# Kernel optimization log

Hardware: AMD Instinct MI355X
Metric: run time of the kernel (lower is better)

Reference implementation:

```python
import jax, jax.numpy as jnp
import numpy as np

N_CHAINS, L, N, D, K, H, FF = 8192, 128, 100000, 256, 8, 4, 1024
LN_EPS = 1e-5  # torch LayerNorm default
EPS = 1e-8     # module eps for mean-pool denom


def _ln(x, g, b):
    mu = jnp.mean(x, axis=-1, keepdims=True)
    var = jnp.mean((x - mu) ** 2, axis=-1, keepdims=True)
    return (x - mu) * jax.lax.rsqrt(var + LN_EPS) * g + b


def setup_inputs() -> dict:
    key = jax.random.key(0)
    ks = jax.random.split(key, 24)
    s = 1.0 / np.sqrt(D)
    inp = {
        "v": jax.random.normal(ks[0], (N, D), jnp.float32),
        "batch_idx": jax.random.randint(ks[1], (N_CHAINS, L), 0, N),
        "mask": jax.random.uniform(ks[2], (N_CHAINS, L)) > 0.5,
        "count": jax.random.randint(ks[3], (N_CHAINS,), 0, 128).astype(jnp.float32),
        "rank_scores": jax.random.normal(ks[4], (N_CHAINS, L), jnp.float32),
        "pos_embed": jnp.zeros((1, K, D), jnp.float32),
        "w_qkv": jax.random.normal(ks[5], (3 * D, D), jnp.float32) * s,
        "b_qkv": jnp.zeros((3 * D,), jnp.float32),
        "w_o": jax.random.normal(ks[6], (D, D), jnp.float32) * s,
        "b_o": jnp.zeros((D,), jnp.float32),
        "ln1_g": jnp.ones((D,), jnp.float32),
        "ln1_b": jnp.zeros((D,), jnp.float32),
        "ln2_g": jnp.ones((D,), jnp.float32),
        "ln2_b": jnp.zeros((D,), jnp.float32),
        "w_ff1": jax.random.normal(ks[7], (FF, D), jnp.float32) * s,
        "b_ff1": jnp.zeros((FF,), jnp.float32),
        "w_ff2": jax.random.normal(ks[8], (D, FF), jnp.float32) / np.sqrt(FF),
        "b_ff2": jnp.zeros((D,), jnp.float32),
        "w_out1": jax.random.normal(ks[9], (FF, D + 1), jnp.float32) * s,
        "b_out1": jnp.zeros((FF,), jnp.float32),
        "w_out2": jax.random.normal(ks[10], (D, FF), jnp.float32) / np.sqrt(FF),
        "b_out2": jnp.zeros((D,), jnp.float32),
    }
    return inp


def reference(v, batch_idx, mask, count, rank_scores, pos_embed, w_qkv, b_qkv,
              w_o, b_o, ln1_g, ln1_b, ln2_g, ln2_b, w_ff1, b_ff1, w_ff2, b_ff2,
              w_out1, b_out1, w_out2, b_out2):
    neg = jnp.finfo(jnp.float32).min
    # --- top-k relevance selection among masked positions ---
    masked_scores = jnp.where(mask, rank_scores.astype(jnp.float32), neg)
    _, top_idx = jax.lax.top_k(masked_scores, K)                # [n, K]
    picked = jnp.take_along_axis(mask, top_idx, axis=1)
    sortable = jnp.where(picked, top_idx, L)                     # sentinel L
    sortable = jnp.sort(sortable, axis=1)
    picked = sortable < L
    safe_idx = jnp.where(picked, sortable, 0)                    # [n, K]
    # gather-pack: v[batch_idx][safe_idx] == v[batch_idx gathered at safe_idx]
    member_idx = jnp.take_along_axis(batch_idx, safe_idx, axis=1)
    packed = v[member_idx] * picked[..., None].astype(v.dtype)   # [n, K, D]

    x = packed + pos_embed[:, :K, :]
    kpm = ~picked                                                # True = pad
    empty = jnp.all(kpm, axis=1)
    kpm = kpm.at[:, 0].set(jnp.where(empty, False, kpm[:, 0]))

    # --- one pre-LN transformer encoder layer (gelu, dropout=0) ---
    dh = D // H
    h = _ln(x, ln1_g, ln1_b)
    qkv = h @ w_qkv.T + b_qkv                                    # [n, K, 3D]
    q, k, val = jnp.split(qkv, 3, axis=-1)
    q = q.reshape(-1, K, H, dh)
    k = k.reshape(-1, K, H, dh)
    val = val.reshape(-1, K, H, dh)
    scores = jnp.einsum('bqhd,bkhd->bhqk', q, k) / np.sqrt(dh)
    scores = jnp.where(kpm[:, None, None, :], neg, scores)
    attn = jax.nn.softmax(scores, axis=-1)
    o = jnp.einsum('bhqk,bkhd->bqhd', attn, val).reshape(-1, K, D)
    x = x + (o @ w_o.T + b_o)
    h = _ln(x, ln2_g, ln2_b)
    x = x + jax.nn.gelu(h @ w_ff1.T + b_ff1, approximate=False) @ w_ff2.T + b_ff2

    # --- masked mean pool + log-count feature + MLP head ---
    pf = picked.astype(x.dtype)
    denom = jnp.clip(jnp.sum(pf, axis=1, keepdims=True), EPS, None)
    pooled = jnp.sum(x * pf[..., None], axis=1) / denom
    pooled = jnp.where(jnp.any(picked, axis=1, keepdims=True), pooled, 0.0)
    feat = jnp.concatenate([pooled, jnp.log1p(count.astype(x.dtype))[:, None]], axis=-1)
    return jax.nn.gelu(feat @ w_out1.T + b_out1, approximate=False) @ w_out2.T + b_out2
```

## Files before the change

kernel.cpp:

```cpp
#include <hip/hip_runtime.h>


#define DIM   256
#define LSEQ  128
#define KTOK  8

typedef __bf16 bf16x8 __attribute__((ext_vector_type(8)));
typedef float  f32x4  __attribute__((ext_vector_type(4)));
typedef unsigned short u16x8 __attribute__((ext_vector_type(8)));

__device__ __forceinline__ f32x4 mfma16(bf16x8 a, bf16x8 b, f32x4 c) {
  return __builtin_amdgcn_mfma_f32_16x16x32_bf16(a, b, c, 0, 0, 0);
}

__device__ __forceinline__ unsigned short f2bf(float f) {
  union { __bf16 h; unsigned short u; } cv;
  cv.h = (__bf16)f;
  return cv.u;
}

__device__ __forceinline__ unsigned pack2bf(float a, float b) {
  union { __bf16 h2[2]; unsigned u; } cv;
  cv.h2[0] = (__bf16)a; cv.h2[1] = (__bf16)b;
  return cv.u;
}

__device__ __forceinline__ float gelu_fast(float x) {
  const float x2 = x * x;
  const float y = x * __builtin_fmaf(0.0356774081f, x2, 0.7978845608f);
  const float e = __expf(2.f * y);
  const float r = __builtin_amdgcn_rcpf(e + 1.f);
  const float t = __builtin_fmaf(-2.f, r, 1.f);
  return 0.5f * x * (1.f + t);
}

__device__ __forceinline__ float rsum8(float v) {
  v += __shfl_xor(v, 1);
  v += __shfl_xor(v, 2);
  v += __shfl_xor(v, 4);
  return v;
}

union U4 { unsigned u[4]; bf16x8 v; };

__device__ __forceinline__ void gload16(const unsigned short* g, unsigned short* lds_uniform) {
  auto gp = reinterpret_cast<const __attribute__((address_space(1))) unsigned*>(
      reinterpret_cast<uintptr_t>(g));
  auto lp = reinterpret_cast<__attribute__((address_space(3))) unsigned*>(
      (unsigned)reinterpret_cast<uintptr_t>(lds_uniform));
  __builtin_amdgcn_global_load_lds(gp, lp, 16, 0, 0);
}

struct Stage32 { u16x8 r[4]; };
__device__ __forceinline__ void stage_load(Stage32& st, const unsigned short* __restrict__ g, int tid) {
  #pragma unroll
  for (int i = 0; i < 4; ++i) st.r[i] = *(const u16x8*)&g[(tid + i * 512) * 8];
}
__device__ __forceinline__ void stage_commit(const Stage32& st, unsigned short* l, int tid) {
  #pragma unroll
  for (int i = 0; i < 4; ++i) *(u16x8*)&l[(tid + i * 512) * 8] = st.r[i];
}

__device__ __forceinline__ void pack_region(
    const float* __restrict__ src, unsigned short* __restrict__ dst,
    int g, int KC, int Ksrc, int Klim)
{
  const int ln = g & 63;
  const int t = g >> 6;
  const int s = t % KC;
  const int ntile = t / KC;
  const int row = ntile * 16 + (ln & 15);
  const int c0 = s * 32 + (ln >> 4) * 8;
  u16x8 o;
  #pragma unroll
  for (int j = 0; j < 8; ++j) {
    float val = (c0 + j < Klim) ? src[(long)row * Ksrc + c0 + j] : 0.f;
    o[j] = f2bf(val);
  }
  *(u16x8*)&dst[(long)g * 8] = o;
}

__device__ __forceinline__ void pack_region_kmaj(
    const float* __restrict__ src, unsigned short* __restrict__ dst,
    int g, int NT, int Ksrc)
{
  const int ln = g & 63;
  const int t = g >> 6;
  const int ntile = t % NT;
  const int s = t / NT;
  const int row = ntile * 16 + (ln & 15);
  const int c0 = s * 32 + (ln >> 4) * 8;
  u16x8 o;
  #pragma unroll
  for (int j = 0; j < 8; ++j) o[j] = f2bf(src[(long)row * Ksrc + c0 + j]);
  *(u16x8*)&dst[(long)g * 8] = o;
}

#define PREP_GROUPS 172032
__global__ __launch_bounds__(256) void k_prep(
    const float* __restrict__ wqkv, const float* __restrict__ wo,
    const float* __restrict__ wff1, const float* __restrict__ wff2,
    const float* __restrict__ wout1, const float* __restrict__ wout2,
    unsigned short* __restrict__ oq, unsigned short* __restrict__ oo,
    unsigned short* __restrict__ of1, unsigned short* __restrict__ of2,
    unsigned short* __restrict__ oo1, unsigned short* __restrict__ oo2)
{
  int g = blockIdx.x * 256 + threadIdx.x;
  if (g < 24576) { pack_region(wqkv, oq, g, 8, 256, 256); return; }
  g -= 24576;
  if (g < 8192)  { pack_region(wo, oo, g, 8, 256, 256); return; }
  g -= 8192;
  if (g < 32768) { pack_region(wff1, of1, g, 8, 256, 256); return; }
  g -= 32768;
  if (g < 32768) { pack_region_kmaj(wff2, of2, g, 16, 1024); return; }
  g -= 32768;
  if (g < 40960) { pack_region(wout1, oo1, g, 10, 257, 257); return; }
  g -= 40960;
  if (g < 32768) { pack_region_kmaj(wout2, oo2, g, 16, 1024); }
}

__global__ __launch_bounds__(256) void k_sel(
    const float* __restrict__ v, const int* __restrict__ batch_idx,
    const int* __restrict__ mask, const float* __restrict__ rank_scores,
    const float* __restrict__ pos_embed,
    const float* __restrict__ ln1g, const float* __restrict__ ln1b,
    float* __restrict__ X, unsigned short* __restrict__ H1p,
    int* __restrict__ NPICK)
{
  const int c = blockIdx.x;
  const int tid = threadIdx.x;
  __shared__ int s_mem[KTOK];
  __shared__ int s_np;

  if (tid < 64) {
    const int l = tid;
    unsigned long long key[2];
    #pragma unroll
    for (int t = 0; t < 2; ++t) {
      int p = l + 64 * t;
      int mk = mask[c * LSEQ + p];
      float s = rank_scores[c * LSEQ + p];
      unsigned u = __float_as_uint(s);
      u = (u & 0x80000000u) ? ~u : (u | 0x80000000u);
      unsigned long long kk =
          ((unsigned long long)u << 32) | (unsigned long long)(0xFFFFFFFFu - (unsigned)p);
      key[t] = mk ? kk : 0ull;
    }
    int w[KTOK];
    #pragma unroll
    for (int r = 0; r < KTOK; ++r) w[r] = 0x7FFFFFFF;
    int np = 0;
    for (int r = 0; r < KTOK; ++r) {
      unsigned long long best = key[0] > key[1] ? key[0] : key[1];
      for (int off = 32; off > 0; off >>= 1) {
        unsigned long long o = __shfl_xor(best, off, 64);
        if (o > best) best = o;
      }
      if (best == 0ull) break;
      int idx = (int)(0xFFFFFFFFu - (unsigned)(best & 0xFFFFFFFFull));
      w[np++] = idx;
      if (key[0] == best) key[0] = 0ull;
      if (key[1] == best) key[1] = 0ull;
    }
    #pragma unroll
    for (int a = 0; a < KTOK - 1; ++a)
      #pragma unroll
      for (int b2 = 0; b2 < KTOK - 1 - a; ++b2) {
        int x0 = w[b2], x1 = w[b2 + 1];
        w[b2] = min(x0, x1); w[b2 + 1] = max(x0, x1);
      }
    if (l < KTOK) s_mem[l] = (l < np) ? batch_idx[c * LSEQ + w[l]] : -1;
    if (l == 0) { s_np = np; NPICK[c] = np; }
  }
  __syncthreads();

  const int np = s_np;
  const int j = tid >> 5, q = tid & 31;
  const int r = s_mem[j];
  const float4* v4  = (const float4*)v;
  const float4* pe4 = (const float4*)pos_embed;
  float4* X4 = (float4*)X;

  float4 xv[2];
  #pragma unroll
  for (int rep = 0; rep < 2; ++rep) {
    const int f = 2 * q + rep;
    float4 pe = pe4[j * 64 + f];
    float4 val = make_float4(0.f, 0.f, 0.f, 0.f);
    if (j < np) val = v4[(long)r * 64 + f];
    xv[rep].x = val.x + pe.x; xv[rep].y = val.y + pe.y;
    xv[rep].z = val.z + pe.z; xv[rep].w = val.w + pe.w;
    X4[((long)c * KTOK + j) * 64 + f] = xv[rep];
  }
  float sum = 0.f, ss = 0.f;
  #pragma unroll
  for (int rep = 0; rep < 2; ++rep) {
    sum += xv[rep].x + xv[rep].y + xv[rep].z + xv[rep].w;
    ss  += xv[rep].x * xv[rep].x + xv[rep].y * xv[rep].y
         + xv[rep].z * xv[rep].z + xv[rep].w * xv[rep].w;
  }
  #pragma unroll
  for (int off = 1; off <= 16; off <<= 1) {
    sum += __shfl_xor(sum, off); ss += __shfl_xor(ss, off);
  }
  const float mu = sum * (1.f / 256.f);
  const float var = ss * (1.f / 256.f) - mu * mu;
  const float rstd = rsqrtf(var + 1e-5f);
  const int t = c * KTOK + j;
  const int mtile = t >> 4, lr = t & 15;
  const int s = q >> 2, lq = q & 3;
  u16x8 o;
  const int col = q * 8;
  o[0] = f2bf((xv[0].x - mu) * rstd * ln1g[col + 0] + ln1b[col + 0]);
  o[1] = f2bf((xv[0].y - mu) * rstd * ln1g[col + 1] + ln1b[col + 1]);
  o[2] = f2bf((xv[0].z - mu) * rstd * ln1g[col + 2] + ln1b[col + 2]);
  o[3] = f2bf((xv[0].w - mu) * rstd * ln1g[col + 3] + ln1b[col + 3]);
  o[4] = f2bf((xv[1].x - mu) * rstd * ln1g[col + 4] + ln1b[col + 4]);
  o[5] = f2bf((xv[1].y - mu) * rstd * ln1g[col + 5] + ln1b[col + 5]);
  o[6] = f2bf((xv[1].z - mu) * rstd * ln1g[col + 6] + ln1b[col + 6]);
  o[7] = f2bf((xv[1].w - mu) * rstd * ln1g[col + 7] + ln1b[col + 7]);
  *(u16x8*)&H1p[((long)(mtile * 8 + s) * 64 + lq * 16 + lr) * 8] = o;
}

__global__ __launch_bounds__(512, 4) void k_qkv(
    const unsigned short* __restrict__ H1p, unsigned short* __restrict__ QKVp,
    const unsigned short* __restrict__ wqp, const float* __restrict__ bqkv)
{
  __shared__ unsigned short buf[16384];
  __shared__ unsigned short sT[8 * 16 * 72];
  const int tid = threadIdx.x;
  const int wv = tid >> 6, ln = tid & 63;
  const int lr = ln & 15, lq = ln >> 4;
  const int mtile = blockIdx.x * 8 + wv;
  const f32x4 vzero = {0.f, 0.f, 0.f, 0.f};
  unsigned short* sTw = &sT[wv * 1152];

  bf16x8 af[8];
  #pragma unroll
  for (int s = 0; s < 8; ++s)
    af[s] = *(const bf16x8*)&H1p[((long)(mtile * 8 + s) * 64 + ln) * 8];

  Stage32 st;
  stage_load(st, wqp, tid);
  for (int c = 0; c < 12; ++c) {
    stage_commit(st, buf, tid);
    __syncthreads();
    if (c < 11) stage_load(st, wqp + (c + 1) * 16384, tid);
    f32x4 acc[4];
    #pragma unroll
    for (int nt = 0; nt < 4; ++nt) acc[nt] = vzero;
    #pragma unroll
    for (int s = 0; s < 8; ++s) {
      #pragma unroll
      for (int nt = 0; nt < 4; ++nt) {
        bf16x8 b = *(const bf16x8*)&buf[(nt * 8 + s) * 512 + ln * 8];
        acc[nt] = mfma16(af[s], b, acc[nt]);
      }
    }
    #pragma unroll
    for (int nt = 0; nt < 4; ++nt) {
      const float bias = bqkv[c * 64 + nt * 16 + lr];
      #pragma unroll
      for (int reg = 0; reg < 4; ++reg)
        sTw[(lq * 4 + reg) * 72 + nt * 16 + lr] = f2bf(acc[nt][reg] + bias);
    }
    const int r8 = ln >> 3, cg = ln & 7;
    #pragma unroll
    for (int h = 0; h < 2; ++h) {
      const int tok = h * 8 + r8;
      u16x8 vv = *(const u16x8*)&sTw[tok * 72 + cg * 8];
      *(u16x8*)&QKVp[((long)(mtile * 16 + tok)) * 768 + c * 64 + cg * 8] = vv;
    }
    __syncthreads();
  }
}

#define SKV 520

__global__ __launch_bounds__(128) void k_attn(
    const unsigned short* __restrict__ QKVp, const int* __restrict__ NPICK,
    unsigned short* __restrict__ Op)
{
  __shared__ unsigned short sKV[32 * SKV];
  __shared__ int s_np[4];
  const int tid = threadIdx.x;
  const int blk = blockIdx.x;
  if (tid < 4) s_np[tid] = NPICK[blk * 4 + tid];
  for (int i = tid; i < 2048; i += 128) {
    const int r = i >> 6, u = i & 63;
    *(u16x8*)&sKV[r * SKV + u * 8] =
        *(const u16x8*)&QKVp[((long)blk * 32 + r) * 768 + 256 + u * 8];
  }
  const int c = tid >> 5, hh = (tid >> 3) & 3, qi = tid & 7;
  const int qrow = c * 8 + qi;
  bf16x8 qv[8];
  #pragma unroll
  for (int dc = 0; dc < 8; ++dc)
    qv[dc] = *(const bf16x8*)&QKVp[((long)blk * 32 + qrow) * 768 + hh * 64 + dc * 8];
  __syncthreads();

  const int natt = max(1, s_np[c]);
  float sc[8];
  #pragma unroll
  for (int j = 0; j < 8; ++j) sc[j] = -1e30f;
  for (int j = 0; j < natt; ++j) {
    float d = 0.f;
    #pragma unroll
    for (int dc = 0; dc < 8; ++dc) {
      bf16x8 kv = *(const bf16x8*)&sKV[(c * 8 + j) * SKV + hh * 64 + dc * 8];
      #pragma unroll
      for (int e = 0; e < 8; ++e) d += (float)qv[dc][e] * (float)kv[e];
    }
    sc[j] = d * 0.125f;
  }
  float mx = -1e30f;
  #pragma unroll
  for (int j = 0; j < 8; ++j) mx = fmaxf(mx, sc[j]);
  float pr[8]; float ssum = 0.f;
  #pragma unroll
  for (int j = 0; j < 8; ++j) {
    float e = (j < natt) ? __expf(sc[j] - mx) : 0.f;
    pr[j] = e; ssum += e;
  }
  const float inv = 1.f / ssum;
  const int t = blk * 32 + qrow;
  const int mt = t >> 4, lrt = t & 15;
  #pragma unroll
  for (int dc = 0; dc < 8; ++dc) {
    float o8[8] = {0.f,0.f,0.f,0.f,0.f,0.f,0.f,0.f};
    for (int j = 0; j < natt; ++j) {
      const float pj = pr[j] * inv;
      bf16x8 vv = *(const bf16x8*)&sKV[(c * 8 + j) * SKV + 256 + hh * 64 + dc * 8];
      #pragma unroll
      for (int e = 0; e < 8; ++e) o8[e] += pj * (float)vv[e];
    }
    u16x8 o;
    #pragma unroll
    for (int e = 0; e < 8; ++e) o[e] = f2bf(o8[e]);
    const int s = hh * 2 + (dc >> 2), lqt = dc & 3;
    *(u16x8*)&Op[((long)(mt * 8 + s) * 64 + lqt * 16 + lrt) * 8] = o;
  }
}

__global__ __launch_bounds__(512, 4) void k_oproj(
    const unsigned short* __restrict__ Op, float* __restrict__ X,
    const unsigned short* __restrict__ wop, const float* __restrict__ bo,
    const float* __restrict__ ln2g, const float* __restrict__ ln2b,
    unsigned short* __restrict__ H2p)
{
  __shared__ unsigned short buf[16384];
  __shared__ float sTf[8 * 16 * 68];
  const int tid = threadIdx.x;
  const int wv = tid >> 6, ln = tid & 63;
  const int lr = ln & 15, lq = ln >> 4;
  const int mtile = blockIdx.x * 8 + wv;
  const f32x4 vzero = {0.f, 0.f, 0.f, 0.f};
  float* sTw = &sTf[wv * 1088];

  bf16x8 af[8];
  #pragma unroll
  for (int s = 0; s < 8; ++s)
    af[s] = *(const bf16x8*)&Op[((long)(mtile * 8 + s) * 64 + ln) * 8];

  const int r4 = ln >> 2, g4 = ln & 3;
  float lsum = 0.f, lss = 0.f;

  Stage32 st;
  stage_load(st, wop, tid);
  for (int c = 0; c < 4; ++c) {
    stage_commit(st, buf, tid);
    __syncthreads();
    if (c < 3) stage_load(st, wop + (c + 1) * 16384, tid);
    f32x4 acc[4];
    #pragma unroll
    for (int nt = 0; nt < 4; ++nt) acc[nt] = vzero;
    #pragma unroll
    for (int s = 0; s < 8; ++s) {
      #pragma unroll
      for (int nt = 0; nt < 4; ++nt) {
        bf16x8 b = *(const bf16x8*)&buf[(nt * 8 + s) * 512 + ln * 8];
        acc[nt] = mfma16(af[s], b, acc[nt]);
      }
    }
    #pragma unroll
    for (int nt = 0; nt < 4; ++nt) {
      const float bias = bo[c * 64 + nt * 16 + lr];
      #pragma unroll
      for (int reg = 0; reg < 4; ++reg)
        sTw[(lq * 4 + reg) * 68 + nt * 16 + lr] = acc[nt][reg] + bias;
    }
    #pragma unroll
    for (int it = 0; it < 4; ++it) {
      const int gi = it * 4 + g4;
      f32x4 vv = *(const f32x4*)&sTw[r4 * 68 + gi * 4];
      float4* xp = (float4*)&X[((long)(mtile * 16 + r4)) * DIM + c * 64 + gi * 4];
      float4 old = *xp;
      old.x += vv[0]; old.y += vv[1]; old.z += vv[2]; old.w += vv[3];
      *xp = old;
      lsum += old.x + old.y + old.z + old.w;
      lss  += old.x * old.x + old.y * old.y + old.z * old.z + old.w * old.w;
    }
    __syncthreads();
  }
  lsum += __shfl_xor(lsum, 1); lss += __shfl_xor(lss, 1);
  lsum += __shfl_xor(lsum, 2); lss += __shfl_xor(lss, 2);
  const float mu = lsum * (1.f / 256.f);
  const float rstd = rsqrtf(lss * (1.f / 256.f) - mu * mu + 1e-5f);
  const int row = mtile * 16 + r4;
  #pragma unroll
  for (int i = 0; i < 8; ++i) {
    const int q = i * 4 + g4;
    const float4 x0 = *(const float4*)&X[(long)row * DIM + q * 8];
    const float4 x1 = *(const float4*)&X[(long)row * DIM + q * 8 + 4];
    const float4 g0 = *(const float4*)&ln2g[q * 8];
    const float4 g1 = *(const float4*)&ln2g[q * 8 + 4];
    const float4 b0 = *(const float4*)&ln2b[q * 8];
    const float4 b1 = *(const float4*)&ln2b[q * 8 + 4];
    u16x8 o;
    o[0] = f2bf((x0.x - mu) * rstd * g0.x + b0.x);
    o[1] = f2bf((x0.y - mu) * rstd * g0.y + b0.y);
    o[2] = f2bf((x0.z - mu) * rstd * g0.z + b0.z);
    o[3] = f2bf((x0.w - mu) * rstd * g0.w + b0.w);
    o[4] = f2bf((x1.x - mu) * rstd * g1.x + b1.x);
    o[5] = f2bf((x1.y - mu) * rstd * g1.y + b1.y);
    o[6] = f2bf((x1.z - mu) * rstd * g1.z + b1.z);
    o[7] = f2bf((x1.w - mu) * rstd * g1.w + b1.w);
    *(u16x8*)&H2p[((long)(mtile * 8 + (q >> 2)) * 64 + (q & 3) * 16 + r4) * 8] = o;
  }
}

__global__ __launch_bounds__(256, 2) void k_ff(
    const float* __restrict__ X, const unsigned short* __restrict__ H2p,
    const unsigned short* __restrict__ w1p, const unsigned short* __restrict__ w2p,
    const float* __restrict__ bff1, const float* __restrict__ bff2,
    const int* __restrict__ NPICK, const float* __restrict__ count,
    unsigned short* __restrict__ Fp)
{
  __shared__ unsigned short buf[2][8192];
  __shared__ unsigned short Gs[16384];
  __shared__ float Pxf[4096];
  const int tid = threadIdx.x;
  const int wv = tid >> 6, ln = tid & 63;
  const int lr = ln & 15, lq = ln >> 4;
  const int blk = blockIdx.x;
  const int mtA = blk * 8 + wv * 2, mtB = mtA + 1;
  const f32x4 vzero = {0.f, 0.f, 0.f, 0.f};

  const int sub = (ln >> 3) & 1;
  const int npcAl = NPICK[mtA * 2 + sub];
  const int npcBl = NPICK[mtB * 2 + sub];
  const float mTA = ((ln & 7) < npcAl) ? 1.f : 0.f;
  const float mTB = ((ln & 7) < npcBl) ? 1.f : 0.f;
  const int chA = wv * 4 + sub;
  const int chB = wv * 4 + 2 + sub;

  bf16x8 afA[8], afB[8];
  #pragma unroll
  for (int s = 0; s < 8; ++s) {
    afA[s] = *(const bf16x8*)&H2p[((long)(mtA * 8 + s) * 64 + ln) * 8];
    afB[s] = *(const bf16x8*)&H2p[((long)(mtB * 8 + s) * 64 + ln) * 8];
  }

  #pragma unroll
  for (int c = 0; c < 4; ++c) {
    const int off = (c * 256 + wv * 64) * 8;
    gload16(w1p + off + ln * 8, &buf[0][off]);
  }
  __syncthreads();

  for (int i = 0; i < 32; ++i) {
    const unsigned short* bcur = buf[i & 1];
    if (i < 31) {
      unsigned short* bnxt = buf[(i + 1) & 1];
      #pragma unroll
      for (int c = 0; c < 4; ++c) {
        const int off = (c * 256 + wv * 64) * 8;
        gload16(w1p + (long)(i + 1) * 8192 + off + ln * 8, &bnxt[off]);
      }
    }
    f32x4 gaA[2], gaB[2];
    #pragma unroll
    for (int nt = 0; nt < 2; ++nt) { gaA[nt] = vzero; gaB[nt] = vzero; }
    #pragma unroll
    for (int s = 0; s < 8; ++s) {
      #pragma unroll
      for (int nt = 0; nt < 2; ++nt) {
        const bf16x8 w1f = *(const bf16x8*)&bcur[(nt * 8 + s) * 512 + ln * 8];
        gaA[nt] = mfma16(w1f, afA[s], gaA[nt]);
        gaB[nt] = mfma16(w1f, afB[s], gaB[nt]);
      }
    }
    float sA[2][4], sB[2][4];
    #pragma unroll
    for (int nt = 0; nt < 2; ++nt) {
      const float4 b4 = *(const float4*)&bff1[i * 32 + nt * 16 + lq * 4];
      sA[nt][0] = rsum8(gelu_fast(gaA[nt][0] + b4.x) * mTA);
      sA[nt][1] = rsum8(gelu_fast(gaA[nt][1] + b4.y) * mTA);
      sA[nt][2] = rsum8(gelu_fast(gaA[nt][2] + b4.z) * mTA);
      sA[nt][3] = rsum8(gelu_fast(gaA[nt][3] + b4.w) * mTA);
      sB[nt][0] = rsum8(gelu_fast(gaB[nt][0] + b4.x) * mTB);
      sB[nt][1] = rsum8(gelu_fast(gaB[nt][1] + b4.y) * mTB);
      sB[nt][2] = rsum8(gelu_fast(gaB[nt][2] + b4.z) * mTB);
      sB[nt][3] = rsum8(gelu_fast(gaB[nt][3] + b4.w) * mTB);
    }
    if ((ln & 7) == 0) {
      #pragma unroll
      for (int nt = 0; nt < 2; ++nt)
        #pragma unroll
        for (int reg = 0; reg < 4; ++reg) {
          const int r = lq * 4 + reg;
          const int pos = (nt * 2 + (r >> 3)) * 16;
          const int e = r & 7;
          Gs[i * 512 + (chA + pos) * 8 + e] = f2bf(sA[nt][reg]);
          Gs[i * 512 + (chB + pos) * 8 + e] = f2bf(sB[nt][reg]);
        }
    }
    __syncthreads();
  }

  #pragma unroll
  for (int grp = 0; grp < 2; ++grp) {
    const int mt = grp ? mtB : mtA;
    const int npc = NPICK[mt * 2 + (lq >> 1)];
    float mk[4];
    #pragma unroll
    for (int reg = 0; reg < 4; ++reg)
      mk[reg] = (((lq * 4 + reg) & 7) < npc) ? 1.f : 0.f;
    #pragma unroll
    for (int nt = 0; nt < 16; ++nt) {
      const int col = nt * 16 + lr;
      float ps = 0.f;
      #pragma unroll
      for (int reg = 0; reg < 4; ++reg)
        ps += mk[reg] * X[((long)mt * 16 + lq * 4 + reg) * DIM + col];
      ps += __shfl_xor(ps, 16);
      if ((lq & 1) == 0)
        Pxf[(wv * 4 + grp * 2 + (lq >> 1)) * 256 + col] = ps;
    }
  }
  __syncthreads();

  f32x4 C[4];
  #pragma unroll
  for (int nt = 0; nt < 4; ++nt) C[nt] = vzero;
  for (int s = 0; s < 32; ++s) {
    const bf16x8 ag = *(const bf16x8*)&Gs[s * 512 + ln * 8];
    #pragma unroll
    for (int nt = 0; nt < 4; ++nt) {
      const bf16x8 w2f =
          *(const bf16x8*)&w2p[((long)(s * 16 + wv * 4 + nt) * 64 + ln) * 8];
      C[nt] = mfma16(ag, w2f, C[nt]);
    }
  }
  #pragma unroll
  for (int nt = 0; nt < 4; ++nt) {
    #pragma unroll
    for (int reg = 0; reg < 4; ++reg) {
      const int m = lq * 4 + reg;
      const int col = wv * 64 + nt * 16 + lr;
      Pxf[m * 256 + col] += C[nt][reg];
    }
  }
  __syncthreads();

  for (int t = tid; t < 640; t += 256) {
    const int ch = t / 40, grp = t % 40;
    const int npc = NPICK[blk * 16 + ch];
    u16x8 o;
    if (grp < 32) {
      const float inv = (npc > 0) ? (1.f / (float)npc) : 0.f;
      const f32x4 p0 = *(const f32x4*)&Pxf[ch * 256 + grp * 8];
      const f32x4 p1 = *(const f32x4*)&Pxf[ch * 256 + grp * 8 + 4];
      const float4 b0 = *(const float4*)&bff2[grp * 8];
      const float4 b1 = *(const float4*)&bff2[grp * 8 + 4];
      if (npc > 0) {
        o[0] = f2bf(p0[0] * inv + b0.x); o[1] = f2bf(p0[1] * inv + b0.y);
        o[2] = f2bf(p0[2] * inv + b0.z); o[3] = f2bf(p0[3] * inv + b0.w);
        o[4] = f2bf(p1[0] * inv + b1.x); o[5] = f2bf(p1[1] * inv + b1.y);
        o[6] = f2bf(p1[2] * inv + b1.z); o[7] = f2bf(p1[3] * inv + b1.w);
      } else {
        #pragma unroll
        for (int j = 0; j < 8; ++j) o[j] = 0;
      }
    } else {
      #pragma unroll
      for (int j = 0; j < 8; ++j) o[j] = 0;
      if (grp == 32) o[0] = f2bf(log1pf(count[blk * 16 + ch]));
    }
    const int s = grp >> 2, lqf = grp & 3;
    *(u16x8*)&Fp[((long)(blk * 10 + s) * 64 + lqf * 16 + ch) * 8] = o;
  }
}

__global__ __launch_bounds__(512, 4) void k_headmlp(
    const unsigned short* __restrict__ Fp,
    const unsigned short* __restrict__ wo1p, const unsigned short* __restrict__ wo2p,
    const float* __restrict__ bout1, const float* __restrict__ bout2,
    float* __restrict__ out)
{
  __shared__ unsigned short bufA[20480];
  __shared__ unsigned short bufB[16384];
  const int tid = threadIdx.x;
  const int fq = blockIdx.x & 3;
  const int mchunk = blockIdx.x >> 2;
  const int wv = tid >> 6, ln = tid & 63;
  const int lr = ln & 15, lq = ln >> 4;
  const int rtile = mchunk * 8 + wv;
  const f32x4 vzero = {0.f, 0.f, 0.f, 0.f};

  f32x4 oacc[16];
  #pragma unroll
  for (int nt = 0; nt < 16; ++nt) oacc[nt] = vzero;

  const int laneA = ((lq & 1) * 2) * 16 + lr;
  const int laneB = laneA + 16;
  const bool hi = (lq & 2) != 0;

  for (int it = 0; it < 4; ++it) {
    const int f = fq * 4 + it;
    __syncthreads();
    #pragma unroll
    for (int i = 0; i < 5; ++i) {
      const int off = (i * 512 + wv * 64) * 8;
      gload16(wo1p + (long)f * 20480 + off + ln * 8, &bufA[off]);
    }
    #pragma unroll
    for (int i = 0; i < 4; ++i) {
      const int off = (i * 512 + wv * 64) * 8;
      gload16(wo2p + (long)f * 16384 + off + ln * 8, &bufB[off]);
    }
    __syncthreads();

    f32x4 ga[4];
    #pragma unroll
    for (int nt = 0; nt < 4; ++nt) ga[nt] = vzero;
    #pragma unroll
    for (int s = 0; s < 10; ++s) {
      const bf16x8 afs = *(const bf16x8*)&Fp[((long)(rtile * 10 + s) * 64 + ln) * 8];
      #pragma unroll
      for (int nt = 0; nt < 4; ++nt) {
        bf16x8 w1f = *(const bf16x8*)&bufA[(nt * 10 + s) * 512 + ln * 8];
        ga[nt] = mfma16(w1f, afs, ga[nt]);
      }
    }
    unsigned p0[4], p1[4];
    #pragma unroll
    for (int nt = 0; nt < 4; ++nt) {
      const float4 b4 = *(const float4*)&bout1[f * 64 + nt * 16 + lq * 4];
      const float g0 = gelu_fast(ga[nt][0] + b4.x);
      const float g1 = gelu_fast(ga[nt][1] + b4.y);
      const float g2 = gelu_fast(ga[nt][2] + b4.z);
      const float g3 = gelu_fast(ga[nt][3] + b4.w);
      p0[nt] = pack2bf(g0, g1);
      p1[nt] = pack2bf(g2, g3);
    }
    #pragma unroll
    for (int s2 = 0; s2 < 2; ++s2) {
      const unsigned a0 = (unsigned)__shfl((int)p0[2 * s2],     laneA, 64);
      const unsigned a1 = (unsigned)__shfl((int)p1[2 * s2],     laneA, 64);
      const unsigned a2 = (unsigned)__shfl((int)p0[2 * s2],     laneB, 64);
      const unsigned a3 = (unsigned)__shfl((int)p1[2 * s2],     laneB, 64);
      const unsigned c0 = (unsigned)__shfl((int)p0[2 * s2 + 1], laneA, 64);
      const unsigned c1 = (unsigned)__shfl((int)p1[2 * s2 + 1], laneA, 64);
      const unsigned c2 = (unsigned)__shfl((int)p0[2 * s2 + 1], laneB, 64);
      const unsigned c3 = (unsigned)__shfl((int)p1[2 * s2 + 1], laneB, 64);
      U4 uu;
      uu.u[0] = hi ? c0 : a0; uu.u[1] = hi ? c1 : a1;
      uu.u[2] = hi ? c2 : a2; uu.u[3] = hi ? c3 : a3;
      const bf16x8 gfrag = uu.v;
      #pragma unroll
      for (int nt = 0; nt < 16; ++nt) {
        bf16x8 w2f = *(const bf16x8*)&bufB[(s2 * 16 + nt) * 512 + ln * 8];
        oacc[nt] = mfma16(gfrag, w2f, oacc[nt]);
      }
    }
  }
  #pragma unroll
  for (int nt = 0; nt < 16; ++nt) {
    const int col = nt * 16 + lr;
    const float bias = (fq == 0) ? bout2[col] : 0.f;
    #pragma unroll
    for (int reg = 0; reg < 4; ++reg) {
      const int row = mchunk * 128 + wv * 16 + lq * 4 + reg;
      atomicAdd(&out[(long)row * DIM + col], oacc[nt][reg] + bias);
    }
  }
}

extern "C" void kernel_launch(void* const* d_in, const int* in_sizes, int n_in,
                              void* d_out, int out_size, void* d_ws, size_t ws_size,
                              hipStream_t stream) {
  (void)in_sizes; (void)n_in; (void)out_size; (void)ws_size;
  const float* v          = (const float*)d_in[0];
  const int*   batch_idx  = (const int*)  d_in[1];
  const int*   mask       = (const int*)  d_in[2];
  const float* count      = (const float*)d_in[3];
  const float* rank       = (const float*)d_in[4];
  const float* pe         = (const float*)d_in[5];
  const float* w_qkv      = (const float*)d_in[6];
  const float* b_qkv      = (const float*)d_in[7];
  const float* w_o        = (const float*)d_in[8];
  const float* b_o        = (const float*)d_in[9];
  const float* ln1g       = (const float*)d_in[10];
  const float* ln1b       = (const float*)d_in[11];
  const float* ln2g       = (const float*)d_in[12];
  const float* ln2b       = (const float*)d_in[13];
  const float* w_ff1      = (const float*)d_in[14];
  const float* b_ff1      = (const float*)d_in[15];
  const float* w_ff2      = (const float*)d_in[16];
  const float* b_ff2      = (const float*)d_in[17];
  const float* w_out1     = (const float*)d_in[18];
  const float* b_out1     = (const float*)d_in[19];
  const float* w_out2     = (const float*)d_in[20];
  const float* b_out2     = (const float*)d_in[21];
  float* out = (float*)d_out;

  char* ws = (char*)d_ws;
  float*          X     = (float*)ws;
  unsigned short* H1p   = (unsigned short*)(ws + 67108864);
  unsigned short* Op    = H1p;
  unsigned short* QKVp  = (unsigned short*)(ws + 100663296);
  unsigned short* H2p   = QKVp;
  unsigned short* Fp    = (unsigned short*)(ws + 134217728);
  int*            NPICK = (int*)(ws + 201326592);
  unsigned short* wq_bf   = (unsigned short*)(ws + 201359360);
  unsigned short* wo_bf   = (unsigned short*)(ws + 201752576);
  unsigned short* wff1_bf = (unsigned short*)(ws + 201883648);
  unsigned short* wff2_bf = (unsigned short*)(ws + 202407936);
  unsigned short* wo1_bf  = (unsigned short*)(ws + 202932224);
  unsigned short* wo2_bf  = (unsigned short*)(ws + 203587584);

  k_prep<<<PREP_GROUPS / 256, 256, 0, stream>>>(
      w_qkv, w_o, w_ff1, w_ff2, w_out1, w_out2,
      wq_bf, wo_bf, wff1_bf, wff2_bf, wo1_bf, wo2_bf);

  k_sel<<<8192, 256, 0, stream>>>(v, batch_idx, mask, rank, pe,
                                  ln1g, ln1b, X, H1p, NPICK);

  k_qkv<<<512, 512, 0, stream>>>(H1p, QKVp, wq_bf, b_qkv);

  k_attn<<<2048, 128, 0, stream>>>(QKVp, NPICK, Op);

  k_oproj<<<512, 512, 0, stream>>>(Op, X, wo_bf, b_o, ln2g, ln2b, H2p);

  k_ff<<<512, 256, 0, stream>>>(X, H2p, wff1_bf, wff2_bf, b_ff1, b_ff2,
                                NPICK, count, Fp);

  hipMemsetAsync(out, 0, (size_t)8192 * 256 * sizeof(float), stream);

  k_headmlp<<<256, 512, 0, stream>>>(Fp, wo1_bf, wo2_bf, b_out1, b_out2, out);
}
```

Before: 520.5 us.

## Split FF kernel over hidden halves and move pooling epilogue to separate kernel

The FF kernel now launches twice as many blocks, each processing half of the 1024-wide hidden dimension, which halves per-block shared memory for the gelu buffer and doubles the parallelism. Partial FF2 results per half are written to a global fp32 buffer. A new finalize kernel sums the two partials with the masked residual pool of X, which it loops only over picked tokens, then applies bias and mean scaling and writes the packed bf16 features plus the log-count. This adds an extra launch and a round trip of partials through global memory in exchange for higher occupancy and less redundant X reading.

New measurement: 513.9 us. About the same (-1.3%).

```diff
diff --git a/kernel.cpp b/kernel.cpp
--- a/kernel.cpp
+++ b/kernel.cpp
@@ -430,20 +430,19 @@
 }
 
 __global__ __launch_bounds__(256, 2) void k_ff(
-    const float* __restrict__ X, const unsigned short* __restrict__ H2p,
+    const unsigned short* __restrict__ H2p,
     const unsigned short* __restrict__ w1p, const unsigned short* __restrict__ w2p,
-    const float* __restrict__ bff1, const float* __restrict__ bff2,
-    const int* __restrict__ NPICK, const float* __restrict__ count,
-    unsigned short* __restrict__ Fp)
+    const float* __restrict__ bff1, const int* __restrict__ NPICK,
+    float* __restrict__ Pxg)
 {
   __shared__ unsigned short buf[2][8192];
-  __shared__ unsigned short Gs[16384];
-  __shared__ float Pxf[4096];
+  __shared__ unsigned short Gs[8192];
   const int tid = threadIdx.x;
   const int wv = tid >> 6, ln = tid & 63;
   const int lr = ln & 15, lq = ln >> 4;
-  const int blk = blockIdx.x;
-  const int mtA = blk * 8 + wv * 2, mtB = mtA + 1;
+  const int mb = blockIdx.x >> 1;
+  const int h  = blockIdx.x & 1;
+  const int mtA = mb * 8 + wv * 2, mtB = mtA + 1;
   const f32x4 vzero = {0.f, 0.f, 0.f, 0.f};
 
   const int sub = (ln >> 3) & 1;
@@ -464,18 +463,19 @@
   #pragma unroll
   for (int c = 0; c < 4; ++c) {
     const int off = (c * 256 + wv * 64) * 8;
-    gload16(w1p + off + ln * 8, &buf[0][off]);
+    gload16(w1p + (long)(h * 16) * 8192 + off + ln * 8, &buf[0][off]);
   }
   __syncthreads();
 
-  for (int i = 0; i < 32; ++i) {
+  for (int i = 0; i < 16; ++i) {
+    const int gi = h * 16 + i;
     const unsigned short* bcur = buf[i & 1];
-    if (i < 31) {
+    if (i < 15) {
       unsigned short* bnxt = buf[(i + 1) & 1];
       #pragma unroll
       for (int c = 0; c < 4; ++c) {
         const int off = (c * 256 + wv * 64) * 8;
-        gload16(w1p + (long)(i + 1) * 8192 + off + ln * 8, &bnxt[off]);
+        gload16(w1p + (long)(gi + 1) * 8192 + off + ln * 8, &bnxt[off]);
       }
     }
     f32x4 gaA[2], gaB[2];
@@ -493,7 +493,7 @@
     float sA[2][4], sB[2][4];
     #pragma unroll
     for (int nt = 0; nt < 2; ++nt) {
-      const float4 b4 = *(const float4*)&bff1[i * 32 + nt * 16 + lq * 4];
+      const float4 b4 = *(const float4*)&bff1[gi * 32 + nt * 16 + lq * 4];
       sA[nt][0] = rsum8(gelu_fast(gaA[nt][0] + b4.x) * mTA);
       sA[nt][1] = rsum8(gelu_fast(gaA[nt][1] + b4.y) * mTA);
       sA[nt][2] = rsum8(gelu_fast(gaA[nt][2] + b4.z) * mTA);
@@ -518,37 +518,15 @@
     __syncthreads();
   }
 
-  #pragma unroll
-  for (int grp = 0; grp < 2; ++grp) {
-    const int mt = grp ? mtB : mtA;
-    const int npc = NPICK[mt * 2 + (lq >> 1)];
-    float mk[4];
-    #pragma unroll
-    for (int reg = 0; reg < 4; ++reg)
-      mk[reg] = (((lq * 4 + reg) & 7) < npc) ? 1.f : 0.f;
-    #pragma unroll
-    for (int nt = 0; nt < 16; ++nt) {
-      const int col = nt * 16 + lr;
-      float ps = 0.f;
-      #pragma unroll
-      for (int reg = 0; reg < 4; ++reg)
-        ps += mk[reg] * X[((long)mt * 16 + lq * 4 + reg) * DIM + col];
-      ps += __shfl_xor(ps, 16);
-      if ((lq & 1) == 0)
-        Pxf[(wv * 4 + grp * 2 + (lq >> 1)) * 256 + col] = ps;
-    }
-  }
-  __syncthreads();
-
   f32x4 C[4];
   #pragma unroll
   for (int nt = 0; nt < 4; ++nt) C[nt] = vzero;
-  for (int s = 0; s < 32; ++s) {
+  for (int s = 0; s < 16; ++s) {
     const bf16x8 ag = *(const bf16x8*)&Gs[s * 512 + ln * 8];
     #pragma unroll
     for (int nt = 0; nt < 4; ++nt) {
       const bf16x8 w2f =
-          *(const bf16x8*)&w2p[((long)(s * 16 + wv * 4 + nt) * 64 + ln) * 8];
+          *(const bf16x8*)&w2p[((long)((h * 16 + s) * 16 + wv * 4 + nt) * 64 + ln) * 8];
       C[nt] = mfma16(ag, w2f, C[nt]);
     }
   }
@@ -558,37 +536,61 @@
     for (int reg = 0; reg < 4; ++reg) {
       const int m = lq * 4 + reg;
       const int col = wv * 64 + nt * 16 + lr;
-      Pxf[m * 256 + col] += C[nt][reg];
-    }
-  }
-  __syncthreads();
-
-  for (int t = tid; t < 640; t += 256) {
-    const int ch = t / 40, grp = t % 40;
-    const int npc = NPICK[blk * 16 + ch];
-    u16x8 o;
-    if (grp < 32) {
-      const float inv = (npc > 0) ? (1.f / (float)npc) : 0.f;
-      const f32x4 p0 = *(const f32x4*)&Pxf[ch * 256 + grp * 8];
-      const f32x4 p1 = *(const f32x4*)&Pxf[ch * 256 + grp * 8 + 4];
-      const float4 b0 = *(const float4*)&bff2[grp * 8];
-      const float4 b1 = *(const float4*)&bff2[grp * 8 + 4];
-      if (npc > 0) {
-        o[0] = f2bf(p0[0] * inv + b0.x); o[1] = f2bf(p0[1] * inv + b0.y);
-        o[2] = f2bf(p0[2] * inv + b0.z); o[3] = f2bf(p0[3] * inv + b0.w);
-        o[4] = f2bf(p1[0] * inv + b1.x); o[5] = f2bf(p1[1] * inv + b1.y);
-        o[6] = f2bf(p1[2] * inv + b1.z); o[7] = f2bf(p1[3] * inv + b1.w);
-      } else {
-        #pragma unroll
-        for (int j = 0; j < 8; ++j) o[j] = 0;
-      }
-    } else {
-      #pragma unroll
-      for (int j = 0; j < 8; ++j) o[j] = 0;
-      if (grp == 32) o[0] = f2bf(log1pf(count[blk * 16 + ch]));
-    }
-    const int s = grp >> 2, lqf = grp & 3;
-    *(u16x8*)&Fp[((long)(blk * 10 + s) * 64 + lqf * 16 + ch) * 8] = o;
+      Pxg[((long)h * 8192 + mb * 16 + m) * 256 + col] = C[nt][reg];
+    }
+  }
+}
+
+__global__ __launch_bounds__(256) void k_fin(
+    const float* __restrict__ X, const float* __restrict__ Pxg,
+    const float* __restrict__ bff2, const int* __restrict__ NPICK,
+    const float* __restrict__ count, unsigned short* __restrict__ Fp)
+{
+  const int tid = threadIdx.x, blk = blockIdx.x;
+  const int cl = tid >> 5, t32 = tid & 31;
+  const int ch = blk * 8 + cl;
+  const int np = NPICK[ch];
+  const int rtile = ch >> 4, lrf = ch & 15;
+
+  float s[8] = {0.f,0.f,0.f,0.f,0.f,0.f,0.f,0.f};
+  for (int j = 0; j < np; ++j) {
+    const float4 x0 = *(const float4*)&X[((long)ch * 8 + j) * 256 + t32 * 8];
+    const float4 x1 = *(const float4*)&X[((long)ch * 8 + j) * 256 + t32 * 8 + 4];
+    s[0] += x0.x; s[1] += x0.y; s[2] += x0.z; s[3] += x0.w;
+    s[4] += x1.x; s[5] += x1.y; s[6] += x1.z; s[7] += x1.w;
+  }
+  const float4 c00 = *(const float4*)&Pxg[((long)ch) * 256 + t32 * 8];
+  const float4 c01 = *(const float4*)&Pxg[((long)ch) * 256 + t32 * 8 + 4];
+  const float4 c10 = *(const float4*)&Pxg[((long)(8192 + ch)) * 256 + t32 * 8];
+  const float4 c11 = *(const float4*)&Pxg[((long)(8192 + ch)) * 256 + t32 * 8 + 4];
+  const float4 b0 = *(const float4*)&bff2[t32 * 8];
+  const float4 b1 = *(const float4*)&bff2[t32 * 8 + 4];
+  u16x8 o;
+  if (np > 0) {
+    const float inv = 1.f / (float)np;
+    o[0] = f2bf((s[0] + c00.x + c10.x) * inv + b0.x);
+    o[1] = f2bf((s[1] + c00.y + c10.y) * inv + b0.y);
+    o[2] = f2bf((s[2] + c00.z + c10.z) * inv + b0.z);
+    o[3] = f2bf((s[3] + c00.w + c10.w) * inv + b0.w);
+    o[4] = f2bf((s[4] + c01.x + c11.x) * inv + b1.x);
+    o[5] = f2bf((s[5] + c01.y + c11.y) * inv + b1.y);
+    o[6] = f2bf((s[6] + c01.z + c11.z) * inv + b1.z);
+    o[7] = f2bf((s[7] + c01.w + c11.w) * inv + b1.w);
+  } else {
+    #pragma unroll
+    for (int j = 0; j < 8; ++j) o[j] = 0;
+  }
+  const int sgrp = t32 >> 2, lqf = t32 & 3;
+  *(u16x8*)&Fp[((long)(rtile * 10 + sgrp) * 64 + lqf * 16 + lrf) * 8] = o;
+
+  if (tid < 64) {
+    const int ch2 = blk * 8 + (tid >> 3);
+    const int grp = 32 + (tid & 7);
+    const int rt2 = ch2 >> 4, lr2 = ch2 & 15;
+    u16x8 oz = {0,0,0,0,0,0,0,0};
+    if (grp == 32) oz[0] = f2bf(log1pf(count[ch2]));
+    const int s2 = grp >> 2, lq2 = grp & 3;
+    *(u16x8*)&Fp[((long)(rt2 * 10 + s2) * 64 + lq2 * 16 + lr2) * 8] = oz;
   }
 }
 
@@ -719,6 +721,7 @@
   float*          X     = (float*)ws;
   unsigned short* H1p   = (unsigned short*)(ws + 67108864);
   unsigned short* Op    = H1p;
+  float*          Pxg   = (float*)(ws + 67108864);
   unsigned short* QKVp  = (unsigned short*)(ws + 100663296);
   unsigned short* H2p   = QKVp;
   unsigned short* Fp    = (unsigned short*)(ws + 134217728);
@@ -743,8 +746,9 @@
 
   k_oproj<<<512, 512, 0, stream>>>(Op, X, wo_bf, b_o, ln2g, ln2b, H2p);
 
-  k_ff<<<512, 256, 0, stream>>>(X, H2p, wff1_bf, wff2_bf, b_ff1, b_ff2,
-                                NPICK, count, Fp);
+  k_ff<<<1024, 256, 0, stream>>>(H2p, wff1_bf, wff2_bf, b_ff1, NPICK, Pxg);
+
+  k_fin<<<1024, 256, 0, stream>>>(X, Pxg, b_ff2, NPICK, count, Fp);
 
   hipMemsetAsync(out, 0, (size_t)8192 * 256 * sizeof(float), stream);
 
```
